# Kernel optimization log

Hardware: AMD Instinct MI355X
Metric: run time of the kernel (lower is better)

## Reference

```python
import jax, jax.numpy as jnp
import numpy as np

B, T, K = 512, 512, 128
START, STOP = K - 2, K - 1
NEG = -10000.0


def setup_inputs() -> dict:
    key = jax.random.key(0)
    k1, k2, k3, k4 = jax.random.split(key, 4)
    feats = jax.random.normal(k1, (B, T, K), dtype=jnp.float32)
    transitions = jax.random.normal(k2, (K, K), dtype=jnp.float32)
    # CRF.__init__ clamps transitions INTO the start tag and OUT of the stop tag
    transitions = transitions.at[START, :].set(NEG).at[:, STOP].set(NEG)
    tags = jax.random.randint(k3, (B, T), 0, K - 2, dtype=jnp.int32)
    lengths = jax.random.randint(k4, (B,), 1, T + 1, dtype=jnp.int32)
    return {"feats": feats, "transitions": transitions, "tags": tags, "lengths": lengths}


def _forward_alg(feats, trans, lengths):
    # feats: [B, T, K]
    Bb, Tt, Kk = feats.shape
    alpha0 = jnp.full((Bb, Kk), NEG, dtype=feats.dtype).at[:, START].set(0.0)

    def step(alpha, emit):
        # tag_var[b, j, k] = emit[b, j] + trans[j, k] + alpha[b, k]
        tag_var = emit[:, :, None] + trans[None, :, :] + alpha[:, None, :]
        new = jax.nn.logsumexp(tag_var, axis=2)  # stable max + log-sum-exp
        return new, new

    _, alphas = jax.lax.scan(step, alpha0, jnp.swapaxes(feats, 0, 1))  # [T, B, K]
    alphas_all = jnp.concatenate([alpha0[None], alphas], axis=0)       # [T+1, B, K]
    # pick forward_var at position lengths[b] (original indexes [b, lens_[b], :])
    fv = alphas_all[lengths, jnp.arange(Bb)]                            # [B, K]
    terminal = fv + trans[STOP][None, :]
    return jax.nn.logsumexp(terminal, axis=1)                           # [B]


def _score_sentence(feats, trans, tags, lengths):
    Bb, Tt, Kk = feats.shape
    pos = jnp.arange(Tt)
    valid = pos[None, :] < lengths[:, None]                             # [B, T]
    # pad_stop_tags: tags with positions >= len replaced by STOP, then STOP appended
    tags_stop = jnp.where(valid, tags, STOP)
    pad_stop = jnp.concatenate(
        [tags_stop, jnp.full((Bb, 1), STOP, dtype=tags.dtype)], axis=1)  # [B, T+1]
    pad_start = jnp.concatenate(
        [jnp.full((Bb, 1), START, dtype=tags.dtype), tags], axis=1)     # [B, T+1]
    trans_terms = trans[pad_stop, pad_start]                            # [B, T+1]
    tmask = jnp.arange(Tt + 1)[None, :] <= lengths[:, None]             # i in [0, len]
    tscore = jnp.sum(jnp.where(tmask, trans_terms, 0.0), axis=1)
    emit = jnp.take_along_axis(feats, tags[:, :, None].astype(jnp.int32), axis=2)[:, :, 0]
    escore = jnp.sum(jnp.where(valid, emit, 0.0), axis=1)
    return tscore + escore                                              # [B]


def reference(feats, transitions, tags, lengths):
    forward_score = _forward_alg(feats, transitions, lengths)
    gold_score = _score_sentence(feats, transitions, tags, lengths)
    return jnp.mean(jnp.abs(forward_score - gold_score))
```

## Files before the change

kernel.cpp:

```cpp
#include <hip/hip_runtime.h>
#include <math.h>

#define KK 128
#define TT 512
#define BB 512
#define TAG_START 126
#define TAG_STOP 127

typedef float v4f __attribute__((ext_vector_type(4)));

#define XIDX(r) ((r) + (((r) >> 5) << 3))

__device__ __forceinline__ float quad_add(float x, int ctrl) {
    int yi;
    if (ctrl == 0xB1)
        yi = __builtin_amdgcn_update_dpp(0, __float_as_int(x), 0xB1, 0xF, 0xF, true);
    else
        yi = __builtin_amdgcn_update_dpp(0, __float_as_int(x), 0x4E, 0xF, 0xF, true);
    return x + __int_as_float(yi);
}


__global__ __launch_bounds__(512) void order_kernel(const int* __restrict__ lengths,
                                                    int* __restrict__ order) {
    __shared__ int L[BB];
    int tid = threadIdx.x;
    L[tid] = lengths[tid];
    __syncthreads();
    int mylen = L[tid];
    int r = 0;
    for (int i = 0; i < BB; i++) {
        int li = L[i];
        r += (li > mylen) || (li == mylen && i < tid);
    }
    order[r] = tid;
}

__global__ __launch_bounds__(512, 4) void fused_kernel(
    const float* __restrict__ feats, const float* __restrict__ trans,
    const int* __restrict__ tags, const int* __restrict__ lengths,
    const int* __restrict__ order,
    float* __restrict__ fwd_out, float* __restrict__ gold_out) {
    int tid = threadIdx.x;

    if (blockIdx.x < BB) {
        int b = order[blockIdx.x];
        int w = tid >> 6;
        int l = tid & 63;
        int kq = l & 3;
        int row = 16 * w + (l >> 2);

        __shared__ __align__(16) float xs[2][160];
        __shared__ float As[2];
        __shared__ float redm[8], reds[8];

        const float* tp = trans + row * KK + 32 * kq;
        v4f tv[8];
#pragma unroll
        for (int q = 0; q < 8; q++) {
            asm volatile("global_load_dwordx4 %0, %1, off"
                         : "=v"(tv[q]) : "v"(tp + 4 * q));
        }
        int len = lengths[b];
        const float* fbr = feats + (size_t)b * TT * KK + row;
        asm volatile("s_waitcnt vmcnt(0)"
                     : "+v"(tv[0]), "+v"(tv[1]), "+v"(tv[2]), "+v"(tv[3]),
                       "+v"(tv[4]), "+v"(tv[5]), "+v"(tv[6]), "+v"(tv[7]));

        float m32 = -1e30f;
#pragma unroll
        for (int q = 0; q < 8; q++)
            m32 = fmaxf(m32, fmaxf(fmaxf(tv[q].x, tv[q].y), fmaxf(tv[q].z, tv[q].w)));
        m32 = fmaxf(m32, __shfl_xor(m32, 1));
        float Mj = fmaxf(m32, __shfl_xor(m32, 2));

        float Erow[32];
#pragma unroll
        for (int q = 0; q < 8; q++) {
            Erow[4 * q + 0] = __expf(tv[q].x - Mj);
            Erow[4 * q + 1] = __expf(tv[q].y - Mj);
            Erow[4 * q + 2] = __expf(tv[q].z - Mj);
            Erow[4 * q + 3] = __expf(tv[q].w - Mj);
        }

        if (kq == 0) xs[0][XIDX(row)] = (row == TAG_START) ? 1.0f : 0.0f;
        if (tid == 0) { As[0] = 0.f; As[1] = 0.f; }

        float alpha = 0.f, A = 0.f;
        float emb[8];
#pragma unroll
        for (int d = 0; d < 8; d++) {
            int tf = (d < len) ? d : (len - 1);
            emb[d] = fbr[(size_t)tf * KK];
        }
        __syncthreads();

        int tmax = (len + 7) & ~7;
        for (int t0 = 0; t0 < tmax; t0 += 8) {
#pragma unroll
            for (int d = 0; d < 8; d++) {
                int t = t0 + d;
                if (t < len) {
                    float em = emb[d];
                    int tf = (t + 8 < len) ? (t + 8) : (len - 1);
                    emb[d] = fbr[(size_t)tf * KK];

                    int cur = t & 1, nxt = cur ^ 1;
                    float Sn = As[nxt];
                    float fac = __expf(em + Mj + A - Sn);
                    const v4f* x4 = (const v4f*)(xs[cur] + 40 * kq);
                    float s0 = 0.f, s1 = 0.f, s2 = 0.f, s3 = 0.f;
#pragma unroll
                    for (int q = 0; q < 8; q++) {
                        v4f xv = x4[q];
                        s0 = fmaf(Erow[4 * q + 0], xv.x, s0);
                        s1 = fmaf(Erow[4 * q + 1], xv.y, s1);
                        s2 = fmaf(Erow[4 * q + 2], xv.z, s2);
                        s3 = fmaf(Erow[4 * q + 3], xv.w, s3);
                    }
                    float yq = (s0 + s1) + (s2 + s3);
                    yq = quad_add(yq, 0xB1);
                    float y = quad_add(yq, 0x4E);
                    if (kq == 0) xs[nxt][XIDX(row)] = y * fac;
                    alpha = em + Mj + A + __logf(y);
                    if (tid == 0) As[cur] = alpha;
                    A = Sn;
                    __syncthreads();
                }
            }
        }

        float term = (kq == 0) ? (alpha + trans[TAG_STOP * KK + row]) : -1e30f;
        float m = term;
#pragma unroll
        for (int off = 32; off >= 1; off >>= 1) m = fmaxf(m, __shfl_xor(m, off));
        float s = (kq == 0) ? __expf(term - m) : 0.f;
#pragma unroll
        for (int off = 32; off >= 1; off >>= 1) s += __shfl_xor(s, off);
        if (l == 0) { redm[w] = m; reds[w] = s; }
        __syncthreads();
        if (tid == 0) {
            float M2 = redm[0];
            for (int i = 1; i < 8; i++) M2 = fmaxf(M2, redm[i]);
            float S2 = 0.f;
            for (int i = 0; i < 8; i++) S2 += reds[i] * __expf(redm[i] - M2);
            fwd_out[b] = M2 + __logf(S2);
        }
    } else {
        int b = blockIdx.x - BB;
        int len = lengths[b];
        const int* tg = tags + (size_t)b * TT;
        const float* fb = feats + (size_t)b * TT * KK;
        float acc = 0.f;
        for (int i = tid; i <= len; i += 512) {
            int from = (i == 0) ? TAG_START : tg[i - 1];
            int to = (i < len) ? tg[i] : TAG_STOP;
            acc += trans[to * KK + from];
        }
        for (int t = tid; t < len; t += 512)
            acc += fb[(size_t)t * KK + tg[t]];
        __shared__ float sred[8];
#pragma unroll
        for (int off = 32; off >= 1; off >>= 1) acc += __shfl_xor(acc, off);
        if ((tid & 63) == 0) sred[tid >> 6] = acc;
        __syncthreads();
        if (tid == 0) {
            float s = 0.f;
            for (int i = 0; i < 8; i++) s += sred[i];
            gold_out[b] = s;
        }
    }
}

__global__ __launch_bounds__(512) void final_kernel(const float* __restrict__ fwd_s,
                                                    const float* __restrict__ gold_s,
                                                    float* __restrict__ out) {
    int tid = threadIdx.x;
    float v = fabsf(fwd_s[tid] - gold_s[tid]);
#pragma unroll
    for (int off = 32; off >= 1; off >>= 1) v += __shfl_xor(v, off);
    __shared__ float sred[8];
    if ((tid & 63) == 0) sred[tid >> 6] = v;
    __syncthreads();
    if (tid == 0) {
        float s = 0.f;
        for (int i = 0; i < 8; i++) s += sred[i];
        out[0] = s / (float)BB;
    }
}

extern "C" void kernel_launch(void* const* d_in, const int* in_sizes, int n_in,
                              void* d_out, int out_size, void* d_ws, size_t ws_size,
                              hipStream_t stream) {
    const float* feats = (const float*)d_in[0];
    const float* trans = (const float*)d_in[1];
    const int* tags = (const int*)d_in[2];
    const int* lengths = (const int*)d_in[3];

    float* ws = (float*)d_ws;
    float* fwdv = ws;
    float* goldv = ws + BB;
    int* order = (int*)(ws + 2 * BB);

    order_kernel<<<1, 512, 0, stream>>>(lengths, order);
    fused_kernel<<<2 * BB, 512, 0, stream>>>(feats, trans, tags, lengths, order,
                                             fwdv, goldv);
    final_kernel<<<1, 512, 0, stream>>>(fwdv, goldv, (float*)d_out);
}
```

Before: 362.3 us.

## Remap forward recurrence so each lane computes four rows over an eight-column slice

Changes the thread-to-work mapping of the sequential forward recurrence. Each 16-lane group now handles four transition rows, and each lane covers eight columns. Every step needs only two LDS vector reads of the state instead of eight, with 4-step DPP row reductions in place of 2-step quad reductions. Emission loads become float4 per group and the prefetch depth drops from 8 to 4. The trade is more cross-lane reduction work per step and per-step exp/log work concentrated in one lane of each group.

Result: slower. 566.4 us (+56.3%).

```diff
diff --git a/kernel.cpp b/kernel.cpp
--- a/kernel.cpp
+++ b/kernel.cpp
@@ -9,15 +9,20 @@
 
 typedef float v4f __attribute__((ext_vector_type(4)));
 
-#define XIDX(r) ((r) + (((r) >> 5) << 3))
-
-__device__ __forceinline__ float quad_add(float x, int ctrl) {
-    int yi;
-    if (ctrl == 0xB1)
-        yi = __builtin_amdgcn_update_dpp(0, __float_as_int(x), 0xB1, 0xF, 0xF, true);
-    else
-        yi = __builtin_amdgcn_update_dpp(0, __float_as_int(x), 0x4E, 0xF, 0xF, true);
+#define XI(k) ((k) + (((k) >> 5) << 2))
+#define XLEN 144
+
+template <int CTRL>
+__device__ __forceinline__ float dpp_add(float x) {
+    int yi = __builtin_amdgcn_update_dpp(0, __float_as_int(x), CTRL, 0xF, 0xF, true);
     return x + __int_as_float(yi);
+}
+__device__ __forceinline__ float sum16(float x) {
+    x = dpp_add<0xB1>(x);
+    x = dpp_add<0x4E>(x);
+    x = dpp_add<0x140>(x);
+    x = dpp_add<0x128>(x);
+    return x;
 }
 
 
@@ -47,94 +52,131 @@
         int b = order[blockIdx.x];
         int w = tid >> 6;
         int l = tid & 63;
-        int kq = l & 3;
-        int row = 16 * w + (l >> 2);
-
-        __shared__ __align__(16) float xs[2][160];
-        __shared__ float As[2];
+        int c = l & 15;
+        int g = l >> 4;
+        int r0 = 16 * w + 4 * g;
+
+        __shared__ __align__(16) float xs[2][XLEN];
+        __shared__ float As2[2];
         __shared__ float redm[8], reds[8];
 
-        const float* tp = trans + row * KK + 32 * kq;
         v4f tv[8];
 #pragma unroll
-        for (int q = 0; q < 8; q++) {
-            asm volatile("global_load_dwordx4 %0, %1, off"
-                         : "=v"(tv[q]) : "v"(tp + 4 * q));
+        for (int r = 0; r < 4; r++) {
+            const float* tp = trans + (r0 + r) * KK + 8 * c;
+            asm volatile("global_load_dwordx4 %0, %1, off" : "=v"(tv[2 * r]) : "v"(tp));
+            asm volatile("global_load_dwordx4 %0, %1, off" : "=v"(tv[2 * r + 1]) : "v"(tp + 4));
         }
         int len = lengths[b];
-        const float* fbr = feats + (size_t)b * TT * KK + row;
+        const float* fbr4 = feats + (size_t)b * TT * KK + r0;
         asm volatile("s_waitcnt vmcnt(0)"
                      : "+v"(tv[0]), "+v"(tv[1]), "+v"(tv[2]), "+v"(tv[3]),
                        "+v"(tv[4]), "+v"(tv[5]), "+v"(tv[6]), "+v"(tv[7]));
 
-        float m32 = -1e30f;
-#pragma unroll
-        for (int q = 0; q < 8; q++)
-            m32 = fmaxf(m32, fmaxf(fmaxf(tv[q].x, tv[q].y), fmaxf(tv[q].z, tv[q].w)));
-        m32 = fmaxf(m32, __shfl_xor(m32, 1));
-        float Mj = fmaxf(m32, __shfl_xor(m32, 2));
-
-        float Erow[32];
-#pragma unroll
-        for (int q = 0; q < 8; q++) {
-            Erow[4 * q + 0] = __expf(tv[q].x - Mj);
-            Erow[4 * q + 1] = __expf(tv[q].y - Mj);
-            Erow[4 * q + 2] = __expf(tv[q].z - Mj);
-            Erow[4 * q + 3] = __expf(tv[q].w - Mj);
-        }
-
-        if (kq == 0) xs[0][XIDX(row)] = (row == TAG_START) ? 1.0f : 0.0f;
-        if (tid == 0) { As[0] = 0.f; As[1] = 0.f; }
-
-        float alpha = 0.f, A = 0.f;
-        float emb[8];
-#pragma unroll
-        for (int d = 0; d < 8; d++) {
-            int tf = (d < len) ? d : (len - 1);
-            emb[d] = fbr[(size_t)tf * KK];
+        float Mj[4];
+#pragma unroll
+        for (int r = 0; r < 4; r++) {
+            v4f a = tv[2 * r], bv = tv[2 * r + 1];
+            float m = fmaxf(fmaxf(fmaxf(a.x, a.y), fmaxf(a.z, a.w)),
+                            fmaxf(fmaxf(bv.x, bv.y), fmaxf(bv.z, bv.w)));
+            m = fmaxf(m, __shfl_xor(m, 1));
+            m = fmaxf(m, __shfl_xor(m, 2));
+            m = fmaxf(m, __shfl_xor(m, 4));
+            m = fmaxf(m, __shfl_xor(m, 8));
+            Mj[r] = m;
+        }
+        v4f Ev[8];
+#pragma unroll
+        for (int i = 0; i < 8; i++) {
+            float m = Mj[i >> 1];
+            Ev[i].x = __expf(tv[i].x - m);
+            Ev[i].y = __expf(tv[i].y - m);
+            Ev[i].z = __expf(tv[i].z - m);
+            Ev[i].w = __expf(tv[i].w - m);
+        }
+
+        if (tid < KK) xs[0][XI(tid)] = (tid == TAG_START) ? 1.0f : 0.0f;
+        if (tid == 0) { As2[0] = 0.f; As2[1] = 0.f; }
+
+        float A = 0.f;
+        float al[4] = {0.f, 0.f, 0.f, 0.f};
+        float4 emb[4];
+        if (c == 0) {
+#pragma unroll
+            for (int d = 0; d < 4; d++) {
+                int tf = (d < len) ? d : (len - 1);
+                emb[d] = *(const float4*)(fbr4 + (size_t)tf * KK);
+            }
         }
         __syncthreads();
 
-        int tmax = (len + 7) & ~7;
-        for (int t0 = 0; t0 < tmax; t0 += 8) {
-#pragma unroll
-            for (int d = 0; d < 8; d++) {
+        int xbase = XI(8 * c);
+        int wbase = XI(r0);
+        int tmax = (len + 3) & ~3;
+        for (int t0 = 0; t0 < tmax; t0 += 4) {
+#pragma unroll
+            for (int d = 0; d < 4; d++) {
                 int t = t0 + d;
                 if (t < len) {
-                    float em = emb[d];
-                    int tf = (t + 8 < len) ? (t + 8) : (len - 1);
-                    emb[d] = fbr[(size_t)tf * KK];
-
                     int cur = t & 1, nxt = cur ^ 1;
-                    float Sn = As[nxt];
-                    float fac = __expf(em + Mj + A - Sn);
-                    const v4f* x4 = (const v4f*)(xs[cur] + 40 * kq);
-                    float s0 = 0.f, s1 = 0.f, s2 = 0.f, s3 = 0.f;
-#pragma unroll
-                    for (int q = 0; q < 8; q++) {
-                        v4f xv = x4[q];
-                        s0 = fmaf(Erow[4 * q + 0], xv.x, s0);
-                        s1 = fmaf(Erow[4 * q + 1], xv.y, s1);
-                        s2 = fmaf(Erow[4 * q + 2], xv.z, s2);
-                        s3 = fmaf(Erow[4 * q + 3], xv.w, s3);
+                    float Sn = As2[nxt];
+                    const v4f* xp = (const v4f*)(xs[cur] + xbase);
+                    v4f xa = xp[0], xb = xp[1];
+                    float y[4];
+#pragma unroll
+                    for (int r = 0; r < 4; r++) {
+                        v4f e0 = Ev[2 * r], e1 = Ev[2 * r + 1];
+                        float p = e0.x * xa.x;
+                        float q = e0.y * xa.y;
+                        p = fmaf(e0.z, xa.z, p);
+                        q = fmaf(e0.w, xa.w, q);
+                        p = fmaf(e1.x, xb.x, p);
+                        q = fmaf(e1.y, xb.y, q);
+                        p = fmaf(e1.z, xb.z, p);
+                        q = fmaf(e1.w, xb.w, q);
+                        y[r] = p + q;
                     }
-                    float yq = (s0 + s1) + (s2 + s3);
-                    yq = quad_add(yq, 0xB1);
-                    float y = quad_add(yq, 0x4E);
-                    if (kq == 0) xs[nxt][XIDX(row)] = y * fac;
-                    alpha = em + Mj + A + __logf(y);
-                    if (tid == 0) As[cur] = alpha;
+#pragma unroll
+                    for (int r = 0; r < 4; r++) y[r] = sum16(y[r]);
+
+                    if (c == 0) {
+                        float4 em = emb[d];
+                        int tf = (t + 4 < len) ? (t + 4) : (len - 1);
+                        emb[d] = *(const float4*)(fbr4 + (size_t)tf * KK);
+                        float b0 = em.x + Mj[0] + A, b1 = em.y + Mj[1] + A;
+                        float b2 = em.z + Mj[2] + A, b3 = em.w + Mj[3] + A;
+                        v4f xn;
+                        xn.x = y[0] * __expf(b0 - Sn);
+                        xn.y = y[1] * __expf(b1 - Sn);
+                        xn.z = y[2] * __expf(b2 - Sn);
+                        xn.w = y[3] * __expf(b3 - Sn);
+                        *(v4f*)(xs[nxt] + wbase) = xn;
+                        al[0] = b0 + __logf(y[0]);
+                        al[1] = b1 + __logf(y[1]);
+                        al[2] = b2 + __logf(y[2]);
+                        al[3] = b3 + __logf(y[3]);
+                        if (tid == 0) As2[cur] = al[0];
+                    }
                     A = Sn;
                     __syncthreads();
                 }
             }
         }
 
-        float term = (kq == 0) ? (alpha + trans[TAG_STOP * KK + row]) : -1e30f;
-        float m = term;
+        float m = -1e30f, s = 0.f;
+        float t0v = 0.f, t1v = 0.f, t2v = 0.f, t3v = 0.f;
+        if (c == 0) {
+            float4 ts = *(const float4*)(trans + TAG_STOP * KK + r0);
+            t0v = al[0] + ts.x;
+            t1v = al[1] + ts.y;
+            t2v = al[2] + ts.z;
+            t3v = al[3] + ts.w;
+            m = fmaxf(fmaxf(t0v, t1v), fmaxf(t2v, t3v));
+        }
 #pragma unroll
         for (int off = 32; off >= 1; off >>= 1) m = fmaxf(m, __shfl_xor(m, off));
-        float s = (kq == 0) ? __expf(term - m) : 0.f;
+        if (c == 0)
+            s = __expf(t0v - m) + __expf(t1v - m) + __expf(t2v - m) + __expf(t3v - m);
 #pragma unroll
         for (int off = 32; off >= 1; off >>= 1) s += __shfl_xor(s, off);
         if (l == 0) { redm[w] = m; reds[w] = s; }
```
